# Kernel optimization log

Measured on AMD Instinct MI355X. Metric: run time of the kernel, lower is better.

## Reference

```python
import jax, jax.numpy as jnp
import numpy as np

N_NODES = 100000

def gcn_conv(x, edge_index, W, b, n_nodes):
    # GCNConv: out = D^{-1/2} (A + I) D^{-1/2} X W + b  (self-loops added)
    src, dst = edge_index[0], edge_index[1]
    loops = jnp.arange(n_nodes, dtype=edge_index.dtype)
    src = jnp.concatenate([src, loops])
    dst = jnp.concatenate([dst, loops])
    deg = jax.ops.segment_sum(jnp.ones_like(dst, dtype=x.dtype), dst, num_segments=n_nodes)
    dinv = jnp.where(deg > 0, jax.lax.rsqrt(deg), 0.0)
    norm = dinv[src] * dinv[dst]  # [E+N]
    h = x @ W  # transform first (small d), then gather/scatter
    msgs = h[src] * norm[:, None]
    out = jax.ops.segment_sum(msgs, dst, num_segments=n_nodes)
    return out + b


def setup_inputs() -> dict:
    key = jax.random.key(0)
    k1, k2, k3, k4, k5, k6 = jax.random.split(key, 6)
    x = jax.random.normal(k1, (N_NODES, 3), dtype=jnp.float32)
    edge_index = jax.random.randint(k2, (2, 2400000), 0, N_NODES, dtype=jnp.int64)
    # Glorot-style init for GCNConv linear weights; zero bias matches PyG default
    W1 = jax.random.normal(k3, (3, 16), dtype=jnp.float32) * (1.0 / np.sqrt(3))
    b1 = jnp.zeros((16,), dtype=jnp.float32)
    W2 = jax.random.normal(k4, (16, 32), dtype=jnp.float32) * (1.0 / np.sqrt(16))
    b2 = jnp.zeros((32,), dtype=jnp.float32)
    return {"x": x, "edge_index": edge_index, "W1": W1, "b1": b1, "W2": W2, "b2": b2}


def reference(x, edge_index, W1, b1, W2, b2):
    n = x.shape[0]
    h = gcn_conv(x, edge_index, W1, b1, n)
    h = jax.nn.relu(h)
    h = gcn_conv(h, edge_index, W2, b2, n)
    # batch is all zeros in the original forward -> single-graph mean pool
    return jnp.mean(h, axis=0, keepdims=True)  # [1, 32]
```

## Files before the change

### kernel.cpp

```cpp
#include <hip/hip_runtime.h>

typedef unsigned int uint;
typedef unsigned long long ull;


#define MAXB  256
#define CAP   16384u
#define BINB  512
#define CHUNK 4096
#define SPL   8
#define AFS   2048.0f
#define AFB   16384
#define AFM   0x1FFFFFu
#define PADN  131072

__device__ __forceinline__ uint slice_lo(uint c, uint s) {
    return (s == 0u) ? 0u : ((c * s / SPL) & ~7u);
}
__device__ __forceinline__ uint slice_hi(uint c, uint s) {
    return (s == SPL - 1u) ? c : ((c * (s + 1u) / SPL) & ~7u);
}

__global__ void __launch_bounds__(BINB)
bin_kernel(const int* __restrict__ key, const int* __restrict__ other,
           uint* __restrict__ cursor, uint* __restrict__ buf, int E) {
    __shared__ uint cnt[MAXB], scanb[MAXB], baseb[MAXB];
    __shared__ uint stage[CHUNK];
    const int tid = threadIdx.x;
    const int e0 = blockIdx.x * CHUNK;
    const int nE = min(CHUNK, E - e0);
    const int my0 = tid * 8;
    const int myc = max(0, min(8, nE - my0));
    if (tid < MAXB) cnt[tid] = 0u;

    uint k8[8], o8[8], r8[8];
    if (myc == 8) {
        int4 ka = ((const int4*)(key + e0))[tid * 2];
        int4 kb = ((const int4*)(key + e0))[tid * 2 + 1];
        int4 oa = ((const int4*)(other + e0))[tid * 2];
        int4 ob = ((const int4*)(other + e0))[tid * 2 + 1];
        k8[0] = ka.x; k8[1] = ka.y; k8[2] = ka.z; k8[3] = ka.w;
        k8[4] = kb.x; k8[5] = kb.y; k8[6] = kb.z; k8[7] = kb.w;
        o8[0] = oa.x; o8[1] = oa.y; o8[2] = oa.z; o8[3] = oa.w;
        o8[4] = ob.x; o8[5] = ob.y; o8[6] = ob.z; o8[7] = ob.w;
    } else {
        for (int r = 0; r < myc; ++r) {
            k8[r] = (uint)key[e0 + my0 + r];
            o8[r] = (uint)other[e0 + my0 + r];
        }
    }
    __syncthreads();
    for (int r = 0; r < myc; ++r) r8[r] = atomicAdd(&cnt[k8[r] >> 9], 1u);
    __syncthreads();
    if (tid < MAXB) scanb[tid] = cnt[tid];
    __syncthreads();
    for (int d = 1; d < MAXB; d <<= 1) {
        uint t = (tid < MAXB && tid >= d) ? scanb[tid - d] : 0u;
        __syncthreads();
        if (tid < MAXB) scanb[tid] += t;
        __syncthreads();
    }
    if (tid < MAXB) baseb[tid] = (uint)tid * CAP + (cnt[tid] ? atomicAdd(&cursor[tid * 16], cnt[tid]) : 0u);
    __syncthreads();
    for (int r = 0; r < myc; ++r) {
        uint b = k8[r] >> 9;
        stage[(scanb[b] - cnt[b]) + r8[r]] = ((k8[r] & 511u) << 17) | o8[r];
    }
    __syncthreads();
    const int wave = tid >> 6, lane = tid & 63;
    for (int b = wave; b < MAXB; b += BINB / 64) {
        uint s0 = scanb[b] - cnt[b], c = cnt[b], gb = baseb[b];
        uint lim = (uint)(b + 1) * CAP;
        for (uint i = lane; i < c; i += 64u) {
            uint gp = gb + i;
            if (gp < lim) buf[gp] = stage[s0 + i];
        }
    }
}

__global__ void __launch_bounds__(1024)
degnode_kernel(const uint* __restrict__ buf, const uint* __restrict__ curD,
               const float* __restrict__ x, uint* __restrict__ degg,
               float* __restrict__ dinv, float4* __restrict__ xd4, int n) {
    __shared__ uint dg[512];
    const int tid = threadIdx.x;
    const int b = blockIdx.x;
    const uint base = (uint)b * CAP;
    const uint c = min(curD[b * 16], CAP);
    if (tid < 512) dg[tid] = 0u;
    __syncthreads();
    for (uint i0 = (uint)tid * 8u; i0 < c; i0 += 8192u) {
        uint cnt8 = min(8u, c - i0);
        uint en[8];
        if (cnt8 == 8u) {
            uint4 a = ((const uint4*)(buf + base + i0))[0];
            uint4 bb = ((const uint4*)(buf + base + i0))[1];
            en[0] = a.x; en[1] = a.y; en[2] = a.z; en[3] = a.w;
            en[4] = bb.x; en[5] = bb.y; en[6] = bb.z; en[7] = bb.w;
        } else {
            for (uint r = 0; r < cnt8; ++r) en[r] = buf[base + i0 + r];
        }
        for (uint r = 0; r < cnt8; ++r) atomicAdd(&dg[en[r] >> 17], 1u);
    }
    __syncthreads();
    if (tid < 512) {
        int node = (b << 9) + tid;
        if (node < n) {
            uint d = dg[tid];
            degg[node] = d;
            float di = rsqrtf((float)(d + 1u));
            dinv[node] = di;
            xd4[node] = make_float4(x[3 * node] * di, x[3 * node + 1] * di,
                                    x[3 * node + 2] * di, di);
        }
    }
}

__global__ void __launch_bounds__(1024)
aggq_kernel(const uint* __restrict__ buf, const uint* __restrict__ curD,
            const uint* __restrict__ degg, const float4* __restrict__ xd4,
            const float* __restrict__ W1, const float* __restrict__ b1,
            uint4* __restrict__ qb, float* __restrict__ T, int n) {
    __shared__ ull acc[512];
    __shared__ float taccs[16];
    const int tid = threadIdx.x;
    const int b = blockIdx.x;
    const uint base = (uint)b * CAP;
    const uint c = min(curD[b * 16], CAP);
    if (tid < 512) acc[tid] = 0ull;
    if (tid < 16) taccs[tid] = 0.0f;
    __syncthreads();
    for (uint i0 = (uint)tid * 8u; i0 < c; i0 += 8192u) {
        uint cnt8 = min(8u, c - i0);
        uint en[8];
        if (cnt8 == 8u) {
            uint4 a = ((const uint4*)(buf + base + i0))[0];
            uint4 bb = ((const uint4*)(buf + base + i0))[1];
            en[0] = a.x; en[1] = a.y; en[2] = a.z; en[3] = a.w;
            en[4] = bb.x; en[5] = bb.y; en[6] = bb.z; en[7] = bb.w;
        } else {
            for (uint r = 0; r < cnt8; ++r) en[r] = buf[base + i0 + r];
            for (uint r = cnt8; r < 8u; ++r) en[r] = en[0];
        }
        float4 gv[8];
#pragma unroll
        for (int r = 0; r < 8; ++r) gv[r] = xd4[en[r] & 0x1FFFFu];
#pragma unroll
        for (uint r = 0; r < 8u; ++r) {
            if (r < cnt8) {
                uint dl = en[r] >> 17;
                ull f0 = (ull)(uint)((int)rintf(gv[r].x * AFS) + AFB);
                ull f1 = (ull)(uint)((int)rintf(gv[r].y * AFS) + AFB);
                ull f2 = (ull)(uint)((int)rintf(gv[r].z * AFS) + AFB);
                atomicAdd(&acc[dl], f0 | (f1 << 21) | (f2 << 42));
            }
        }
    }
    __syncthreads();
    float sq[16];
#pragma unroll
    for (int k = 0; k < 16; ++k) sq[k] = 0.0f;
    if (tid < 512) {
        int node = (b << 9) + tid;
        if (node < n) {
            ull v = acc[tid];
            int ub = (int)(degg[node] * (uint)AFB);
            float4 sv = xd4[node];
            float di = sv.w;
            const float isc = 1.0f / AFS;
            float av = (float)((int)(uint)(v & AFM) - ub) * isc + sv.x;
            float bv = (float)((int)(uint)((v >> 21) & AFM) - ub) * isc + sv.y;
            float cv = (float)((int)(uint)((v >> 42) & AFM) - ub) * isc + sv.z;
            float q[16];
#pragma unroll
            for (int k = 0; k < 16; ++k) {
                float h = di * (av * W1[k] + bv * W1[16 + k] + cv * W1[32 + k]) + b1[k];
                h = fmaxf(h, 0.0f);
                q[k] = di * h;
                sq[k] = di * q[k];
            }
            uint pk[8];
#pragma unroll
            for (int k = 0; k < 8; ++k) {
                uint l = __float_as_uint(q[2 * k]);
                l = (l + 0x7FFFu + ((l >> 16) & 1u)) >> 16;
                uint h2 = __float_as_uint(q[2 * k + 1]);
                h2 = ((h2 + 0x7FFFu + ((h2 >> 16) & 1u)) & 0xFFFF0000u);
                pk[k] = l | h2;
            }
            qb[2 * (size_t)node]     = make_uint4(pk[0], pk[1], pk[2], pk[3]);
            qb[2 * (size_t)node + 1] = make_uint4(pk[4], pk[5], pk[6], pk[7]);
        }
    }
    if (tid < 512) {
#pragma unroll
        for (int k = 0; k < 16; ++k) {
            float v = sq[k];
            for (int off = 32; off > 0; off >>= 1) v += __shfl_down(v, off, 64);
            if ((tid & 63) == 0) atomicAdd(&taccs[k], v);
        }
    }
    __syncthreads();
    if (tid < 16) atomicAdd(&T[tid], taccs[tid]);
}

__global__ void __launch_bounds__(256)
T_kernel(const uint* __restrict__ buf, const uint* __restrict__ curD,
         const float* __restrict__ dinv, const uint4* __restrict__ qb,
         float* __restrict__ T, int n) {
    __shared__ float dt[512];
    __shared__ float tacc[16];
    const int tid = threadIdx.x;
    const int b = blockIdx.x >> 3;
    const uint s = blockIdx.x & 7;
    const uint base = (uint)b * CAP;
    const uint c = min(curD[b * 16], CAP);
    const uint lo = slice_lo(c, s), hi = slice_hi(c, s);
    for (int t = tid; t < 512; t += 256) {
        int node = (b << 9) + t;
        dt[t] = (node < n) ? dinv[node] : 0.0f;
    }
    if (tid < 16) tacc[tid] = 0.0f;
    __syncthreads();
    float rac[16];
#pragma unroll
    for (int k = 0; k < 16; ++k) rac[k] = 0.0f;
    for (uint i0 = lo + (uint)tid * 8u; i0 < hi + 8u * 2048u; i0 += 2048u) {
        if (i0 >= hi) continue;
        uint cnt8 = min(8u, hi - i0);
        uint en[8];
        if (cnt8 == 8u) {
            uint4 a = ((const uint4*)(buf + base + i0))[0];
            uint4 bb = ((const uint4*)(buf + base + i0))[1];
            en[0] = a.x; en[1] = a.y; en[2] = a.z; en[3] = a.w;
            en[4] = bb.x; en[5] = bb.y; en[6] = bb.z; en[7] = bb.w;
        } else {
            for (uint r = 0; r < cnt8; ++r) en[r] = buf[base + i0 + r];
            for (uint r = cnt8; r < 8u; ++r) en[r] = en[0];
        }
        uint4 qa[8], qc[8];
#pragma unroll
        for (int r = 0; r < 8; ++r) {
            uint sv = en[r] & 0x1FFFFu;
            qa[r] = qb[2 * (size_t)sv];
            qc[r] = qb[2 * (size_t)sv + 1];
        }
#pragma unroll
        for (uint r = 0; r < 8u; ++r) {
            if (r < cnt8) {
                float di = dt[en[r] >> 17];
                uint w[8] = {qa[r].x, qa[r].y, qa[r].z, qa[r].w,
                             qc[r].x, qc[r].y, qc[r].z, qc[r].w};
#pragma unroll
                for (int k = 0; k < 8; ++k) {
                    rac[2 * k]     += di * __uint_as_float(w[k] << 16);
                    rac[2 * k + 1] += di * __uint_as_float(w[k] & 0xFFFF0000u);
                }
            }
        }
    }
#pragma unroll
    for (int k = 0; k < 16; ++k) {
        float v = rac[k];
        for (int off = 32; off > 0; off >>= 1) v += __shfl_down(v, off, 64);
        if ((tid & 63) == 0) atomicAdd(&tacc[k], v);
    }
    __syncthreads();
    if (tid < 16) atomicAdd(&T[tid], tacc[tid]);
}

__global__ void out_kernel(const float* __restrict__ T, const float* __restrict__ W2,
                           const float* __restrict__ b2, float* __restrict__ out, float invN) {
    int j = threadIdx.x;
    float s = 0.0f;
#pragma unroll
    for (int k = 0; k < 16; ++k) s += T[k] * W2[k * 32 + j];
    out[j] = b2[j] + invN * s;
}

extern "C" void kernel_launch(void* const* d_in, const int* in_sizes, int n_in,
                              void* d_out, int out_size, void* d_ws, size_t ws_size,
                              hipStream_t stream) {
    const float* x   = (const float*)d_in[0];
    const int*   ei  = (const int*)d_in[1];
    const float* W1  = (const float*)d_in[2];
    const float* b1  = (const float*)d_in[3];
    const float* W2  = (const float*)d_in[4];
    const float* b2  = (const float*)d_in[5];
    float* out = (float*)d_out;

    const int n = in_sizes[0] / 3;
    const int E = in_sizes[1] / 2;
    const int* src = ei;
    const int* dst = ei + E;

    char* p = (char*)d_ws;
    float* T    = (float*)p;    p += 64;
    uint*  curD = (uint*)p;     p += MAXB * 16 * 4;
    size_t zbytes = (size_t)(p - (char*)d_ws);
    uint*  degg  = (uint*)p;    p += (size_t)n * 4;
    uint*  bufD  = (uint*)p;    p += (size_t)MAXB * CAP * 4;
    float* dinv  = (float*)p;   p += (size_t)n * 4;
    p = (char*)(((size_t)p + 31) & ~(size_t)31);
    float4* xd4  = (float4*)p;  p += (size_t)PADN * 16;
    uint4*  qb   = (uint4*)p;   p += (size_t)PADN * 32;

    const int nb = (n + 511) >> 9;

    hipMemsetAsync(d_ws, 0, zbytes, stream);
    bin_kernel<<<(E + CHUNK - 1) / CHUNK, BINB, 0, stream>>>(dst, src, curD, bufD, E);
    degnode_kernel<<<nb, 1024, 0, stream>>>(bufD, curD, x, degg, dinv, xd4, n);
    aggq_kernel<<<nb, 1024, 0, stream>>>(bufD, curD, degg, xd4, W1, b1, qb, T, n);
    T_kernel<<<nb * SPL, 256, 0, stream>>>(bufD, curD, dinv, qb, T, n);
    out_kernel<<<1, 32, 0, stream>>>(T, W2, b2, out, 1.0f / (float)n);
}
```

Measured before the change: 158.7 us.

## Replace second-layer gather with per-node source-weight sums via dual binning

Because the second layer is followed only by a mean pool, its aggregation is rewritten algebraically. Each node's contribution is its scaled first-layer activation times the sum of dinv over its out-neighbours plus its own dinv. The binning kernel now buckets edges by both destination and source, and the fused kernel accumulates the source-side dinv sums in shared memory. This removes the T_kernel pass that gathered 32-byte bf16 rows per edge, along with the qb buffer writes. In exchange, binning does twice the shared-memory atomics, staging and scattered writes, and the fused kernel makes an extra pass over the source-binned edges.

Result: faster. 144.6 us (-8.9%).

```diff
diff --git a/kernel.cpp b/kernel.cpp
--- a/kernel.cpp
+++ b/kernel.cpp
@@ -8,72 +8,91 @@
 #define CAP   16384u
 #define BINB  512
 #define CHUNK 4096
-#define SPL   8
 #define AFS   2048.0f
 #define AFB   16384
 #define AFM   0x1FFFFFu
 #define PADN  131072
 
-__device__ __forceinline__ uint slice_lo(uint c, uint s) {
-    return (s == 0u) ? 0u : ((c * s / SPL) & ~7u);
-}
-__device__ __forceinline__ uint slice_hi(uint c, uint s) {
-    return (s == SPL - 1u) ? c : ((c * (s + 1u) / SPL) & ~7u);
-}
-
 __global__ void __launch_bounds__(BINB)
-bin_kernel(const int* __restrict__ key, const int* __restrict__ other,
-           uint* __restrict__ cursor, uint* __restrict__ buf, int E) {
-    __shared__ uint cnt[MAXB], scanb[MAXB], baseb[MAXB];
-    __shared__ uint stage[CHUNK];
+bin2_kernel(const int* __restrict__ srcI, const int* __restrict__ dstI,
+            uint* __restrict__ curDg, uint* __restrict__ curSg,
+            uint* __restrict__ bufD, uint* __restrict__ bufS, int E) {
+    __shared__ uint cntD[MAXB], scanD[MAXB], baseD[MAXB];
+    __shared__ uint cntS[MAXB], scanS[MAXB], baseS[MAXB];
+    __shared__ uint stageD[CHUNK];
+    __shared__ uint stageS[CHUNK];
     const int tid = threadIdx.x;
     const int e0 = blockIdx.x * CHUNK;
     const int nE = min(CHUNK, E - e0);
     const int my0 = tid * 8;
     const int myc = max(0, min(8, nE - my0));
-    if (tid < MAXB) cnt[tid] = 0u;
-
-    uint k8[8], o8[8], r8[8];
+    if (tid < MAXB) cntD[tid] = 0u; else cntS[tid - MAXB] = 0u;
+
+    uint d8[8], s8[8], rD[8], rS[8];
     if (myc == 8) {
-        int4 ka = ((const int4*)(key + e0))[tid * 2];
-        int4 kb = ((const int4*)(key + e0))[tid * 2 + 1];
-        int4 oa = ((const int4*)(other + e0))[tid * 2];
-        int4 ob = ((const int4*)(other + e0))[tid * 2 + 1];
-        k8[0] = ka.x; k8[1] = ka.y; k8[2] = ka.z; k8[3] = ka.w;
-        k8[4] = kb.x; k8[5] = kb.y; k8[6] = kb.z; k8[7] = kb.w;
-        o8[0] = oa.x; o8[1] = oa.y; o8[2] = oa.z; o8[3] = oa.w;
-        o8[4] = ob.x; o8[5] = ob.y; o8[6] = ob.z; o8[7] = ob.w;
+        int4 ka = ((const int4*)(dstI + e0))[tid * 2];
+        int4 kb = ((const int4*)(dstI + e0))[tid * 2 + 1];
+        int4 oa = ((const int4*)(srcI + e0))[tid * 2];
+        int4 ob = ((const int4*)(srcI + e0))[tid * 2 + 1];
+        d8[0] = ka.x; d8[1] = ka.y; d8[2] = ka.z; d8[3] = ka.w;
+        d8[4] = kb.x; d8[5] = kb.y; d8[6] = kb.z; d8[7] = kb.w;
+        s8[0] = oa.x; s8[1] = oa.y; s8[2] = oa.z; s8[3] = oa.w;
+        s8[4] = ob.x; s8[5] = ob.y; s8[6] = ob.z; s8[7] = ob.w;
     } else {
         for (int r = 0; r < myc; ++r) {
-            k8[r] = (uint)key[e0 + my0 + r];
-            o8[r] = (uint)other[e0 + my0 + r];
-        }
-    }
-    __syncthreads();
-    for (int r = 0; r < myc; ++r) r8[r] = atomicAdd(&cnt[k8[r] >> 9], 1u);
-    __syncthreads();
-    if (tid < MAXB) scanb[tid] = cnt[tid];
+            d8[r] = (uint)dstI[e0 + my0 + r];
+            s8[r] = (uint)srcI[e0 + my0 + r];
+        }
+    }
+    __syncthreads();
+    for (int r = 0; r < myc; ++r) {
+        rD[r] = atomicAdd(&cntD[d8[r] >> 9], 1u);
+        rS[r] = atomicAdd(&cntS[s8[r] >> 9], 1u);
+    }
+    __syncthreads();
+    const int half = tid >> 8;
+    const int li = tid & 255;
+    uint* cn = half ? cntS : cntD;
+    uint* sc = half ? scanS : scanD;
+    sc[li] = cn[li];
     __syncthreads();
     for (int d = 1; d < MAXB; d <<= 1) {
-        uint t = (tid < MAXB && tid >= d) ? scanb[tid - d] : 0u;
+        uint t = (li >= d) ? sc[li - d] : 0u;
         __syncthreads();
-        if (tid < MAXB) scanb[tid] += t;
+        sc[li] += t;
         __syncthreads();
     }
-    if (tid < MAXB) baseb[tid] = (uint)tid * CAP + (cnt[tid] ? atomicAdd(&cursor[tid * 16], cnt[tid]) : 0u);
+    {
+        uint* cur = half ? curSg : curDg;
+        uint* bs = half ? baseS : baseD;
+        bs[li] = (uint)li * CAP + (cn[li] ? atomicAdd(&cur[li * 16], cn[li]) : 0u);
+    }
     __syncthreads();
     for (int r = 0; r < myc; ++r) {
-        uint b = k8[r] >> 9;
-        stage[(scanb[b] - cnt[b]) + r8[r]] = ((k8[r] & 511u) << 17) | o8[r];
+        uint bD = d8[r] >> 9;
+        stageD[(scanD[bD] - cntD[bD]) + rD[r]] = ((d8[r] & 511u) << 17) | s8[r];
+        uint bS = s8[r] >> 9;
+        stageS[(scanS[bS] - cntS[bS]) + rS[r]] = ((s8[r] & 511u) << 17) | d8[r];
     }
     __syncthreads();
     const int wave = tid >> 6, lane = tid & 63;
-    for (int b = wave; b < MAXB; b += BINB / 64) {
-        uint s0 = scanb[b] - cnt[b], c = cnt[b], gb = baseb[b];
-        uint lim = (uint)(b + 1) * CAP;
-        for (uint i = lane; i < c; i += 64u) {
-            uint gp = gb + i;
-            if (gp < lim) buf[gp] = stage[s0 + i];
+    if (wave < 4) {
+        for (int b = wave; b < MAXB; b += 4) {
+            uint s0 = scanD[b] - cntD[b], c = cntD[b], gb = baseD[b];
+            uint lim = (uint)(b + 1) * CAP;
+            for (uint i = lane; i < c; i += 64u) {
+                uint gp = gb + i;
+                if (gp < lim) bufD[gp] = stageD[s0 + i];
+            }
+        }
+    } else {
+        for (int b = wave - 4; b < MAXB; b += 4) {
+            uint s0 = scanS[b] - cntS[b], c = cntS[b], gb = baseS[b];
+            uint lim = (uint)(b + 1) * CAP;
+            for (uint i = lane; i < c; i += 64u) {
+                uint gp = gb + i;
+                if (gp < lim) bufS[gp] = stageS[s0 + i];
+            }
         }
     }
 }
@@ -117,29 +136,51 @@
 }
 
 __global__ void __launch_bounds__(1024)
-aggq_kernel(const uint* __restrict__ buf, const uint* __restrict__ curD,
-            const uint* __restrict__ degg, const float4* __restrict__ xd4,
-            const float* __restrict__ W1, const float* __restrict__ b1,
-            uint4* __restrict__ qb, float* __restrict__ T, int n) {
+aggqT_kernel(const uint* __restrict__ bufD, const uint* __restrict__ curD,
+             const uint* __restrict__ bufS, const uint* __restrict__ curS,
+             const uint* __restrict__ degg, const float* __restrict__ dinv,
+             const float4* __restrict__ xd4, const float* __restrict__ W1,
+             const float* __restrict__ b1, float* __restrict__ T, int n) {
     __shared__ ull acc[512];
+    __shared__ float gl[512];
     __shared__ float taccs[16];
     const int tid = threadIdx.x;
     const int b = blockIdx.x;
     const uint base = (uint)b * CAP;
-    const uint c = min(curD[b * 16], CAP);
-    if (tid < 512) acc[tid] = 0ull;
+    const uint cD = min(curD[b * 16], CAP);
+    const uint cS = min(curS[b * 16], CAP);
+    if (tid < 512) { acc[tid] = 0ull; gl[tid] = 0.0f; }
     if (tid < 16) taccs[tid] = 0.0f;
     __syncthreads();
-    for (uint i0 = (uint)tid * 8u; i0 < c; i0 += 8192u) {
-        uint cnt8 = min(8u, c - i0);
+    for (uint i0 = (uint)tid * 8u; i0 < cS; i0 += 8192u) {
+        uint cnt8 = min(8u, cS - i0);
         uint en[8];
         if (cnt8 == 8u) {
-            uint4 a = ((const uint4*)(buf + base + i0))[0];
-            uint4 bb = ((const uint4*)(buf + base + i0))[1];
+            uint4 a = ((const uint4*)(bufS + base + i0))[0];
+            uint4 bb = ((const uint4*)(bufS + base + i0))[1];
             en[0] = a.x; en[1] = a.y; en[2] = a.z; en[3] = a.w;
             en[4] = bb.x; en[5] = bb.y; en[6] = bb.z; en[7] = bb.w;
         } else {
-            for (uint r = 0; r < cnt8; ++r) en[r] = buf[base + i0 + r];
+            for (uint r = 0; r < cnt8; ++r) en[r] = bufS[base + i0 + r];
+            for (uint r = cnt8; r < 8u; ++r) en[r] = en[0];
+        }
+        float dv[8];
+#pragma unroll
+        for (int r = 0; r < 8; ++r) dv[r] = dinv[en[r] & 0x1FFFFu];
+#pragma unroll
+        for (uint r = 0; r < 8u; ++r)
+            if (r < cnt8) atomicAdd(&gl[en[r] >> 17], dv[r]);
+    }
+    for (uint i0 = (uint)tid * 8u; i0 < cD; i0 += 8192u) {
+        uint cnt8 = min(8u, cD - i0);
+        uint en[8];
+        if (cnt8 == 8u) {
+            uint4 a = ((const uint4*)(bufD + base + i0))[0];
+            uint4 bb = ((const uint4*)(bufD + base + i0))[1];
+            en[0] = a.x; en[1] = a.y; en[2] = a.z; en[3] = a.w;
+            en[4] = bb.x; en[5] = bb.y; en[6] = bb.z; en[7] = bb.w;
+        } else {
+            for (uint r = 0; r < cnt8; ++r) en[r] = bufD[base + i0 + r];
             for (uint r = cnt8; r < 8u; ++r) en[r] = en[0];
         }
         float4 gv[8];
@@ -171,102 +212,23 @@
             float av = (float)((int)(uint)(v & AFM) - ub) * isc + sv.x;
             float bv = (float)((int)(uint)((v >> 21) & AFM) - ub) * isc + sv.y;
             float cv = (float)((int)(uint)((v >> 42) & AFM) - ub) * isc + sv.z;
-            float q[16];
+            float w = gl[tid] + di;
 #pragma unroll
             for (int k = 0; k < 16; ++k) {
                 float h = di * (av * W1[k] + bv * W1[16 + k] + cv * W1[32 + k]) + b1[k];
                 h = fmaxf(h, 0.0f);
-                q[k] = di * h;
-                sq[k] = di * q[k];
-            }
-            uint pk[8];
-#pragma unroll
-            for (int k = 0; k < 8; ++k) {
-                uint l = __float_as_uint(q[2 * k]);
-                l = (l + 0x7FFFu + ((l >> 16) & 1u)) >> 16;
-                uint h2 = __float_as_uint(q[2 * k + 1]);
-                h2 = ((h2 + 0x7FFFu + ((h2 >> 16) & 1u)) & 0xFFFF0000u);
-                pk[k] = l | h2;
-            }
-            qb[2 * (size_t)node]     = make_uint4(pk[0], pk[1], pk[2], pk[3]);
-            qb[2 * (size_t)node + 1] = make_uint4(pk[4], pk[5], pk[6], pk[7]);
-        }
-    }
-    if (tid < 512) {
-#pragma unroll
-        for (int k = 0; k < 16; ++k) {
-            float v = sq[k];
-            for (int off = 32; off > 0; off >>= 1) v += __shfl_down(v, off, 64);
-            if ((tid & 63) == 0) atomicAdd(&taccs[k], v);
-        }
-    }
-    __syncthreads();
-    if (tid < 16) atomicAdd(&T[tid], taccs[tid]);
-}
-
-__global__ void __launch_bounds__(256)
-T_kernel(const uint* __restrict__ buf, const uint* __restrict__ curD,
-         const float* __restrict__ dinv, const uint4* __restrict__ qb,
-         float* __restrict__ T, int n) {
-    __shared__ float dt[512];
-    __shared__ float tacc[16];
-    const int tid = threadIdx.x;
-    const int b = blockIdx.x >> 3;
-    const uint s = blockIdx.x & 7;
-    const uint base = (uint)b * CAP;
-    const uint c = min(curD[b * 16], CAP);
-    const uint lo = slice_lo(c, s), hi = slice_hi(c, s);
-    for (int t = tid; t < 512; t += 256) {
-        int node = (b << 9) + t;
-        dt[t] = (node < n) ? dinv[node] : 0.0f;
-    }
-    if (tid < 16) tacc[tid] = 0.0f;
-    __syncthreads();
-    float rac[16];
-#pragma unroll
-    for (int k = 0; k < 16; ++k) rac[k] = 0.0f;
-    for (uint i0 = lo + (uint)tid * 8u; i0 < hi + 8u * 2048u; i0 += 2048u) {
-        if (i0 >= hi) continue;
-        uint cnt8 = min(8u, hi - i0);
-        uint en[8];
-        if (cnt8 == 8u) {
-            uint4 a = ((const uint4*)(buf + base + i0))[0];
-            uint4 bb = ((const uint4*)(buf + base + i0))[1];
-            en[0] = a.x; en[1] = a.y; en[2] = a.z; en[3] = a.w;
-            en[4] = bb.x; en[5] = bb.y; en[6] = bb.z; en[7] = bb.w;
-        } else {
-            for (uint r = 0; r < cnt8; ++r) en[r] = buf[base + i0 + r];
-            for (uint r = cnt8; r < 8u; ++r) en[r] = en[0];
-        }
-        uint4 qa[8], qc[8];
-#pragma unroll
-        for (int r = 0; r < 8; ++r) {
-            uint sv = en[r] & 0x1FFFFu;
-            qa[r] = qb[2 * (size_t)sv];
-            qc[r] = qb[2 * (size_t)sv + 1];
-        }
-#pragma unroll
-        for (uint r = 0; r < 8u; ++r) {
-            if (r < cnt8) {
-                float di = dt[en[r] >> 17];
-                uint w[8] = {qa[r].x, qa[r].y, qa[r].z, qa[r].w,
-                             qc[r].x, qc[r].y, qc[r].z, qc[r].w};
-#pragma unroll
-                for (int k = 0; k < 8; ++k) {
-                    rac[2 * k]     += di * __uint_as_float(w[k] << 16);
-                    rac[2 * k + 1] += di * __uint_as_float(w[k] & 0xFFFF0000u);
-                }
+                sq[k] = w * (di * h);
             }
         }
     }
 #pragma unroll
     for (int k = 0; k < 16; ++k) {
-        float v = rac[k];
-        for (int off = 32; off > 0; off >>= 1) v += __shfl_down(v, off, 64);
-        if ((tid & 63) == 0) atomicAdd(&tacc[k], v);
-    }
-    __syncthreads();
-    if (tid < 16) atomicAdd(&T[tid], tacc[tid]);
+        float v2 = sq[k];
+        for (int off = 32; off > 0; off >>= 1) v2 += __shfl_down(v2, off, 64);
+        if ((tid & 63) == 0) atomicAdd(&taccs[k], v2);
+    }
+    __syncthreads();
+    if (tid < 16 && taccs[tid] != 0.0f) atomicAdd(&T[tid], taccs[tid]);
 }
 
 __global__ void out_kernel(const float* __restrict__ T, const float* __restrict__ W2,
@@ -297,20 +259,20 @@
     char* p = (char*)d_ws;
     float* T    = (float*)p;    p += 64;
     uint*  curD = (uint*)p;     p += MAXB * 16 * 4;
+    uint*  curS = (uint*)p;     p += MAXB * 16 * 4;
     size_t zbytes = (size_t)(p - (char*)d_ws);
     uint*  degg  = (uint*)p;    p += (size_t)n * 4;
+    float* dinv  = (float*)p;   p += (size_t)n * 4;
     uint*  bufD  = (uint*)p;    p += (size_t)MAXB * CAP * 4;
-    float* dinv  = (float*)p;   p += (size_t)n * 4;
+    uint*  bufS  = (uint*)p;    p += (size_t)MAXB * CAP * 4;
     p = (char*)(((size_t)p + 31) & ~(size_t)31);
     float4* xd4  = (float4*)p;  p += (size_t)PADN * 16;
-    uint4*  qb   = (uint4*)p;   p += (size_t)PADN * 32;
 
     const int nb = (n + 511) >> 9;
 
     hipMemsetAsync(d_ws, 0, zbytes, stream);
-    bin_kernel<<<(E + CHUNK - 1) / CHUNK, BINB, 0, stream>>>(dst, src, curD, bufD, E);
+    bin2_kernel<<<(E + CHUNK - 1) / CHUNK, BINB, 0, stream>>>(src, dst, curD, curS, bufD, bufS, E);
     degnode_kernel<<<nb, 1024, 0, stream>>>(bufD, curD, x, degg, dinv, xd4, n);
-    aggq_kernel<<<nb, 1024, 0, stream>>>(bufD, curD, degg, xd4, W1, b1, qb, T, n);
-    T_kernel<<<nb * SPL, 256, 0, stream>>>(bufD, curD, dinv, qb, T, n);
+    aggqT_kernel<<<nb, 1024, 0, stream>>>(bufD, curD, bufS, curS, degg, dinv, xd4, W1, b1, T, n);
     out_kernel<<<1, 32, 0, stream>>>(T, W2, b2, out, 1.0f / (float)n);
 }
```
